# Kernel tuning notes

Measured on AMD Instinct MI355X. Metric: run time of the kernel, lower is better.

## Reference

```python
import jax, jax.numpy as jnp
import numpy as np

NC = 80          # num_classes
REG_MAX = 16
TOPK = 10
IMG = 640
STRIDES = (8, 16, 32)
EPS = 1e-9


def make_anchors(shapes, strides):
    pts, strs = [], []
    for (h, w), s in zip(shapes, strides):
        sx = jnp.arange(w, dtype=jnp.float32)  # grid_cell_offset = 0.0
        sy = jnp.arange(h, dtype=jnp.float32)
        gy, gx = jnp.meshgrid(sy, sx, indexing='ij')
        pts.append(jnp.stack([gx, gy], -1).reshape(-1, 2))
        strs.append(jnp.full((h * w, 1), float(s), dtype=jnp.float32))
    return jnp.concatenate(pts, 0), jnp.concatenate(strs, 0)  # [A,2], [A,1]


def ciou(box1, box2, eps=1e-7):
    # boxes are xyxy, broadcastable; returns CIoU with last dim squeezed
    b1x1, b1y1, b1x2, b1y2 = jnp.split(box1, 4, -1)
    b2x1, b2y1, b2x2, b2y2 = jnp.split(box2, 4, -1)
    w1, h1 = b1x2 - b1x1, b1y2 - b1y1
    w2, h2 = b2x2 - b2x1, b2y2 - b2y1
    inter = (jnp.clip(jnp.minimum(b1x2, b2x2) - jnp.maximum(b1x1, b2x1), 0.0)
             * jnp.clip(jnp.minimum(b1y2, b2y2) - jnp.maximum(b1y1, b2y1), 0.0))
    union = w1 * h1 + w2 * h2 - inter + eps
    iou = inter / union
    cw = jnp.maximum(b1x2, b2x2) - jnp.minimum(b1x1, b2x1)
    ch = jnp.maximum(b1y2, b2y2) - jnp.minimum(b1y1, b2y1)
    c2 = cw ** 2 + ch ** 2 + eps
    rho2 = ((b2x1 + b2x2 - b1x1 - b1x2) ** 2 + (b2y1 + b2y2 - b1y1 - b1y2) ** 2) / 4.0
    v = (4.0 / np.pi ** 2) * (jnp.arctan(w2 / (h2 + eps)) - jnp.arctan(w1 / (h1 + eps))) ** 2
    alpha = jax.lax.stop_gradient(v / (v - iou + (1.0 + eps)))
    return (iou - (rho2 / c2 + v * alpha))[..., 0]


def bbox_decode(anchor_points, pred_distri):
    # distribution-focal decode: softmax over REG_MAX bins, expectation, dist2bbox
    B, A, _ = pred_distri.shape
    pd = pred_distri.reshape(B, A, 4, REG_MAX)
    proj = jnp.arange(REG_MAX, dtype=jnp.float32)
    dist = jnp.einsum('bacr,r->bac', jax.nn.softmax(pd, -1), proj)  # [B,A,4] ltrb
    lt, rb = dist[..., :2], dist[..., 2:]
    return jnp.concatenate([anchor_points - lt, anchor_points + rb], -1)  # xyxy


def assigner(pd_scores, pd_bboxes, anc_points, gt_labels, gt_bboxes, mask_gt,
             alpha=0.5, beta=6.0):
    # pd_scores [B,A,C] (sigmoid), pd_bboxes [B,A,4], gt_* [B,M,...], mask_gt [B,M,1]
    B, A, C = pd_scores.shape
    M = gt_bboxes.shape[1]
    mask_gt = mask_gt.astype(jnp.float32)
    # anchors whose center lies inside each gt box
    lt = anc_points[None, None, :, :] - gt_bboxes[:, :, None, :2]   # [B,M,A,2]
    rb = gt_bboxes[:, :, None, 2:] - anc_points[None, None, :, :]
    mask_in_gts = (jnp.minimum(lt.min(-1), rb.min(-1)) > EPS).astype(jnp.float32)  # [B,M,A]
    mask = mask_in_gts * mask_gt
    # class score of each anchor at the gt's label
    sc = jnp.take_along_axis(pd_scores[:, None, :, :],
                             gt_labels[:, :, None, None].astype(jnp.int32), axis=-1)[..., 0]  # [B,M,A]
    overlaps = jnp.clip(ciou(gt_bboxes[:, :, None, :], pd_bboxes[:, None, :, :]), 0.0) * mask
    bbox_scores = sc * mask
    align_metric = (bbox_scores ** alpha) * (overlaps ** beta)  # [B,M,A]
    # top-k candidates per gt
    _, idxs = jax.lax.top_k(align_metric, TOPK)                 # [B,M,K]
    valid = jnp.broadcast_to(mask_gt > 0, (B, M, TOPK))
    idxs = jnp.where(valid, idxs, 0)
    cnt = jnp.zeros((B * M, A), jnp.float32).at[
        jnp.arange(B * M)[:, None], idxs.reshape(B * M, TOPK)
    ].add(valid.reshape(B * M, TOPK).astype(jnp.float32)).reshape(B, M, A)
    mask_topk = jnp.where(cnt > 1, 0.0, cnt)
    mask_pos = mask_topk * mask_in_gts * mask_gt               # [B,M,A]
    # resolve anchors assigned to multiple gts by max overlap
    fg = mask_pos.sum(1)                                       # [B,A]
    multi = fg[:, None, :] > 1
    is_max = jax.nn.one_hot(overlaps.argmax(1), M, dtype=jnp.float32).transpose(0, 2, 1)
    mask_pos = jnp.where(multi, is_max, mask_pos)
    fg_mask = mask_pos.sum(1)                                  # [B,A]
    tgt_idx = mask_pos.argmax(1)                               # [B,A]
    # gather targets
    flat = tgt_idx + jnp.arange(B)[:, None] * M
    t_labels = jnp.clip(gt_labels.reshape(-1)[flat], 0)        # [B,A]
    t_bboxes = gt_bboxes.reshape(-1, 4)[flat]                  # [B,A,4]
    t_scores = jax.nn.one_hot(t_labels, C, dtype=jnp.float32) * (fg_mask[..., None] > 0)
    # normalize scores by aligned metric
    am = align_metric * mask_pos
    pos_am = am.max(-1, keepdims=True)                         # [B,M,1]
    pos_ov = (overlaps * mask_pos).max(-1, keepdims=True)      # [B,M,1]
    norm = (am * pos_ov / (pos_am + EPS)).max(1)[..., None]    # [B,A,1]
    return t_bboxes, t_scores * norm, fg_mask > 0


def setup_inputs() -> dict:
    key = jax.random.key(0)
    ks = jax.random.split(key, 9)
    B, M = 16, 32
    inp = {
        'cls0': jax.random.normal(ks[0], (B, NC, 80, 80), jnp.float32),
        'cls1': jax.random.normal(ks[1], (B, NC, 40, 40), jnp.float32),
        'cls2': jax.random.normal(ks[2], (B, NC, 20, 20), jnp.float32),
        'reg0': jax.random.normal(ks[3], (B, 4 * REG_MAX, 80, 80), jnp.float32),
        'reg1': jax.random.normal(ks[4], (B, 4 * REG_MAX, 40, 40), jnp.float32),
        'reg2': jax.random.normal(ks[5], (B, 4 * REG_MAX, 20, 20), jnp.float32),
    }
    cxy = jax.random.uniform(ks[6], (B, M, 2), minval=0.1, maxval=0.9)
    wh = jax.random.uniform(ks[7], (B, M, 2), minval=0.02, maxval=0.25)
    inp['boxes'] = jnp.concatenate([cxy, wh], -1)  # normalized cxcywh
    inp['labels'] = jax.random.randint(ks[8], (B, M), 0, NC)
    return inp


def reference(cls0, cls1, cls2, reg0, reg1, reg2, boxes, labels):
    cls_out, reg_out = [cls0, cls1, cls2], [reg0, reg1, reg2]
    B = cls0.shape[0]
    anc, stride_t = make_anchors([r.shape[2:] for r in reg_out], STRIDES)
    pred_scores = jnp.concatenate(
        [c.transpose(0, 2, 3, 1).reshape(B, -1, NC) for c in cls_out], 1)        # [B,A,C]
    pred_distri = jnp.concatenate(
        [r.transpose(0, 2, 3, 1).reshape(B, -1, 4 * REG_MAX) for r in reg_out], 1)
    # gt2xyxy: normalized cxcywh -> pixel xyxy
    cx, cy, w, h = jnp.split(boxes, 4, -1)
    gt_bboxes = jnp.concatenate([(cx - w / 2) * IMG, (cy - h / 2) * IMG,
                                 (cx + w / 2) * IMG, (cy + h / 2) * IMG], -1)
    mask_gt = gt_bboxes.sum(2, keepdims=True) > 0.0
    pred_bboxes = bbox_decode(anc, pred_distri)                                   # anchor units
    sg = jax.lax.stop_gradient
    t_bboxes, t_scores, fg_mask = assigner(
        sg(jax.nn.sigmoid(pred_scores)), sg(pred_bboxes) * stride_t,
        anc * stride_t, labels, gt_bboxes, mask_gt)
    tss = jnp.maximum(t_scores.sum(), 1.0)
    # classification BCE-with-logits
    x, t = pred_scores, t_scores
    bce = jnp.maximum(x, 0.0) - x * t + jnp.log1p(jnp.exp(-jnp.abs(x)))
    l_cls = bce.sum() / tss
    # bbox CIoU loss
    t_bboxes = t_bboxes / stride_t
    weight = t_scores.sum(-1) * fg_mask                                           # [B,A]
    iou = ciou(pred_bboxes, t_bboxes)
    l_iou = ((1.0 - iou) * weight).sum() / tss
    # DFL loss
    tltrb = jnp.clip(jnp.concatenate([anc - t_bboxes[..., :2],
                                      t_bboxes[..., 2:] - anc], -1),
                     0.0, REG_MAX - 1 - 0.01)                                     # [B,A,4]
    logp = jax.nn.log_softmax(pred_distri.reshape(B, -1, 4, REG_MAX), -1)
    tl = jnp.floor(tltrb).astype(jnp.int32)
    wl = (tl + 1).astype(jnp.float32) - tltrb
    lp_tl = jnp.take_along_axis(logp, tl[..., None], -1)[..., 0]
    lp_tr = jnp.take_along_axis(logp, (tl + 1)[..., None], -1)[..., 0]
    dfl = (-(lp_tl * wl + lp_tr * (1.0 - wl))).mean(-1)                           # [B,A]
    l_dfl = (dfl * weight).sum() / tss
    loss = jnp.stack([0.5 * l_cls, 7.5 * l_iou, 1.5 * l_dfl])
    return loss.sum(), loss
```

## Files before the change

### kernel.cpp

```cpp
#include <hip/hip_runtime.h>

#define NB 16
#define NM 32
#define NA 8400
#define NCC 80
#define NREG 64
#define A0 6400
#define A1 1600
#define A2 400
#define CAP 768

#define DEC_BLKS 2100
#define BCE_BLKS 2048
#define PRE_GRID (DEC_BLKS + BCE_BLKS)
#define PL_GRID 525


__device__ __forceinline__ void anch(int a, float& ax, float& ay, float& s, int& lvl, int& p) {
  if (a < A0)            { lvl = 0; p = a;          s = 8.f;  ax = (float)(p % 80); ay = (float)(p / 80); }
  else if (a < A0 + A1)  { lvl = 1; p = a - A0;     s = 16.f; ax = (float)(p % 40); ay = (float)(p / 40); }
  else                   { lvl = 2; p = a - A0 - A1; s = 32.f; ax = (float)(p % 20); ay = (float)(p / 20); }
}

__device__ __forceinline__ float cls_at(const float* c0, const float* c1, const float* c2,
                                        int b, int ch, int a) {
  if (a < A0)           return c0[((size_t)(b * NCC + ch)) * A0 + a];
  if (a < A0 + A1)      return c1[((size_t)(b * NCC + ch)) * A1 + (a - A0)];
  return c2[((size_t)(b * NCC + ch)) * A2 + (a - A0 - A1)];
}

__device__ __forceinline__ float reg_at(const float* r0, const float* r1, const float* r2,
                                        int b, int ch, int lvl, int p) {
  if (lvl == 0) return r0[((size_t)(b * NREG + ch)) * A0 + p];
  if (lvl == 1) return r1[((size_t)(b * NREG + ch)) * A1 + p];
  return r2[((size_t)(b * NREG + ch)) * A2 + p];
}

__device__ __forceinline__ void gtbox(const float* boxes, int b, int m,
                                      float& x1, float& y1, float& x2, float& y2, bool& valid) {
  const float* q = boxes + ((size_t)(b * NM + m)) * 4;
  float cx = q[0], cy = q[1], w = q[2], h = q[3];
  x1 = (cx - w * 0.5f) * 640.f; y1 = (cy - h * 0.5f) * 640.f;
  x2 = (cx + w * 0.5f) * 640.f; y2 = (cy + h * 0.5f) * 640.f;
  valid = (x1 + y1 + x2 + y2) > 0.f;
}

__device__ __forceinline__ float ciou_f(float b1x1, float b1y1, float b1x2, float b1y2,
                                        float b2x1, float b2y1, float b2x2, float b2y2) {
  const float eps = 1e-7f;
  float w1 = b1x2 - b1x1, h1 = b1y2 - b1y1;
  float w2 = b2x2 - b2x1, h2 = b2y2 - b2y1;
  float iw = fmaxf(fminf(b1x2, b2x2) - fmaxf(b1x1, b2x1), 0.f);
  float ih = fmaxf(fminf(b1y2, b2y2) - fmaxf(b1y1, b2y1), 0.f);
  float inter = iw * ih;
  float uni = w1 * h1 + w2 * h2 - inter + eps;
  float iou = inter / uni;
  float cw = fmaxf(b1x2, b2x2) - fminf(b1x1, b2x1);
  float ch = fmaxf(b1y2, b2y2) - fminf(b1y1, b2y1);
  float c2 = cw * cw + ch * ch + eps;
  float dx = b2x1 + b2x2 - b1x1 - b1x2;
  float dy = b2y1 + b2y2 - b1y1 - b1y2;
  float rho2 = (dx * dx + dy * dy) * 0.25f;
  float at = atanf(w2 / (h2 + eps)) - atanf(w1 / (h1 + eps));
  float v = 0.4052847345693511f * at * at;
  float alpha = v / (v - iou + (1.0f + eps));
  return iou - (rho2 / c2 + v * alpha);
}

__device__ __forceinline__ float align_of(float sc, float o) {
  float o2 = o * o, o4 = o2 * o2;
  return sqrtf(sc) * (o2 * o4);
}

__device__ __forceinline__ float softplus_fast(float x) {
  float e = __expf(-fabsf(x));
  return fmaxf(x, 0.f) + __logf(1.f + e);
}


__global__ __launch_bounds__(256) void k_pre2(
    const float* r0, const float* r1, const float* r2,
    const float* c0, const float* c1, const float* c2,
    float* bbf, float* mlsf, int* fgcnt, int* msum,
    unsigned* pos_am, unsigned* pos_ov, double* gt_acc, double* bce_part) {
  __shared__ double sred[256];
  if (blockIdx.x < DEC_BLKS) {
    const int g = blockIdx.x * 256 + threadIdx.x;
    if (g < NB * NA) { fgcnt[g] = 0; msum[g] = 0; }
    if (g < NB * NM) { pos_am[g] = 0u; pos_ov[g] = 0u; }
    if (g < NB * NM * 4) gt_acc[g] = 0.0;

    const int BA = NB * NA;
    const int sd = g / BA;
    const int t  = g - sd * BA;
    int b = t / NA, a = t - (t / NA) * NA;
    float ax, ay, s; int lvl, p;
    anch(a, ax, ay, s, lvl, p);
    const float* rg; int HW;
    if (lvl == 0) { rg = r0; HW = A0; }
    else if (lvl == 1) { rg = r1; HW = A1; }
    else { rg = r2; HW = A2; }
    const float* base = rg + ((size_t)(b * NREG + sd * 16)) * HW + p;
    float xv[16];
#pragma unroll
    for (int r = 0; r < 16; ++r) xv[r] = base[(size_t)r * HW];
    float mx = xv[0];
#pragma unroll
    for (int r = 1; r < 16; ++r) mx = fmaxf(mx, xv[r]);
    float se = 0.f, ws = 0.f;
#pragma unroll
    for (int r = 0; r < 16; ++r) { float e = __expf(xv[r] - mx); se += e; ws += e * (float)r; }
    float dist = ws / se;
    float ml = mx + __logf(se);
    float v;
    if (sd == 0)      v = ax - dist;
    else if (sd == 1) v = ay - dist;
    else if (sd == 2) v = ax + dist;
    else              v = ay + dist;
    bbf[(size_t)t * 4 + sd]  = v;
    mlsf[(size_t)t * 4 + sd] = ml;
  } else {
    const int bce_blk = blockIdx.x - DEC_BLKS;
    const size_t N0 = (size_t)NB * NCC * A0 / 4;
    const size_t N1 = (size_t)NB * NCC * A1 / 4;
    const size_t N2 = (size_t)NB * NCC * A2 / 4;
    const size_t NT = N0 + N1 + N2;
    const float4* f0 = (const float4*)c0;
    const float4* f1 = (const float4*)c1;
    const float4* f2 = (const float4*)c2;
    const size_t i0 = (size_t)bce_blk * 256 + threadIdx.x;
    const size_t stride = (size_t)BCE_BLKS * 256;
    float s0 = 0.f, s1 = 0.f;
    for (size_t i = i0; i < NT; i += stride) {
      float4 v;
      if (i < N0) v = f0[i];
      else if (i < N0 + N1) v = f1[i - N0];
      else v = f2[i - N0 - N1];
      s0 += softplus_fast(v.x) + softplus_fast(v.z);
      s1 += softplus_fast(v.y) + softplus_fast(v.w);
    }
    sred[threadIdx.x] = (double)(s0 + s1);
    __syncthreads();
    for (int off = 128; off; off >>= 1) {
      if (threadIdx.x < off) sred[threadIdx.x] += sred[threadIdx.x + off];
      __syncthreads();
    }
    if (threadIdx.x == 0) bce_part[bce_blk] = sred[0];
  }
}


__global__ __launch_bounds__(256) void k_assign(
    const float* boxes, const int* labels, const float4* bb,
    const float* c0, const float* c1, const float* c2,
    int* fgcnt, int* msum) {
  __shared__ float sv[CAP];
  __shared__ int   si[CAP];
  __shared__ int   s_n;
  const int bm = blockIdx.x;
  const int b = bm / NM, m = bm % NM;
  const int tid = threadIdx.x;
  const int lane = tid & 63;

  float gx1, gy1, gx2, gy2; bool valid;
  gtbox(boxes, b, m, gx1, gy1, gx2, gy2, valid);
  if (!valid) return;
  int lbl = labels[bm]; if (lbl < 0) lbl = 0; if (lbl >= NCC) lbl = NCC - 1;
  if (tid == 0) s_n = 0;
  __syncthreads();

  const int   Ws[3]   = {80, 40, 20};
  const float ss[3]   = {8.f, 16.f, 32.f};
  const int   loff[3] = {0, A0, A0 + A1};
  int rx0[3], ry0[3], rw[3], bc[3];
  int total = 0;
  for (int l = 0; l < 3; ++l) {
    float s = ss[l]; int W = Ws[l];
    int ax0 = (int)floorf((gx1 + 1e-9f) / s);
    int ax1 = (int)ceilf((gx2 - 1e-9f) / s);
    int ay0 = (int)floorf((gy1 + 1e-9f) / s);
    int ay1 = (int)ceilf((gy2 - 1e-9f) / s);
    ax0 = max(ax0, 0); ay0 = max(ay0, 0);
    ax1 = min(ax1, W - 1); ay1 = min(ay1, W - 1);
    rx0[l] = ax0; ry0[l] = ay0;
    rw[l] = max(0, ax1 - ax0 + 1);
    int rhl = max(0, ay1 - ay0 + 1);
    bc[l] = total;
    total += rw[l] * rhl;
  }
  int iters = (total + 255) >> 8;
  for (int it = 0; it < iters; ++it) {
    int idx = it * 256 + tid;
    bool pred = false; float am = 0.f; int a = 0;
    if (idx < total) {
      int l = (idx >= bc[2]) ? 2 : ((idx >= bc[1]) ? 1 : 0);
      int r = idx - bc[l];
      int iy = r / rw[l], ix = r - iy * rw[l];
      int axg = rx0[l] + ix, ayg = ry0[l] + iy;
      a = loff[l] + ayg * Ws[l] + axg;
      float s = ss[l];
      float axp = (float)axg * s, ayp = (float)ayg * s;
      float mn = fminf(fminf(axp - gx1, ayp - gy1), fminf(gx2 - axp, gy2 - ayp));
      if (mn > 1e-9f) {
        pred = true;
        float4 pb = bb[(size_t)b * NA + a];
        float c = ciou_f(gx1, gy1, gx2, gy2, pb.x * s, pb.y * s, pb.z * s, pb.w * s);
        float o = fmaxf(c, 0.f);
        float x = cls_at(c0, c1, c2, b, lbl, a);
        float sc = 1.f / (1.f + expf(-x));
        am = align_of(sc, o);
      }
    }
    unsigned long long mask = __ballot(pred);
    if (mask) {
      int nact = __popcll(mask);
      int leader = __ffsll(mask) - 1;
      int basec = 0;
      if (lane == leader) basec = atomicAdd(&s_n, nact);
      basec = __shfl(basec, leader);
      if (pred) {
        int off = basec + __popcll(mask & ((1ull << lane) - 1ull));
        if (off < CAP) { sv[off] = am; si[off] = a; }
      }
    }
  }
  __syncthreads();
  int n = s_n; if (n > CAP) n = CAP;
  if (n == 0) return;
  if (tid >= 64) return;

  float v[12]; int ix[12];
#pragma unroll
  for (int k = 0; k < 12; ++k) {
    int j = k * 64 + tid;
    bool in = (j < n);
    v[k]  = in ? sv[j] : -2.f;
    ix[k] = in ? si[j] : (1 << 30);
  }
  int cnt = 0;
#pragma unroll
  for (int k = 0; k < 12; ++k) cnt += (v[k] > 0.f) ? 1 : 0;
  for (int o = 32; o; o >>= 1) cnt += __shfl_xor(cnt, o);
  int npos = cnt;

  if (npos > 10) {
    for (int p = 0; p < 10; ++p) {
      float bv = -1.f; int bi = 1 << 30;
#pragma unroll
      for (int k = 0; k < 12; ++k) {
        if (v[k] > bv || (v[k] == bv && ix[k] < bi)) { bv = v[k]; bi = ix[k]; }
      }
      for (int o = 32; o; o >>= 1) {
        float wv = __shfl_xor(bv, o); int wi = __shfl_xor(bi, o);
        if (wv > bv || (wv == bv && wi < bi)) { bv = wv; bi = wi; }
      }
#pragma unroll
      for (int k = 0; k < 12; ++k) if (ix[k] == bi) v[k] = -1.f;
      if (tid == 0) {
        atomicAdd(&fgcnt[(size_t)b * NA + bi], 1);
        atomicAdd(&msum[(size_t)b * NA + bi], m);
      }
    }
  } else {
#pragma unroll
    for (int k = 0; k < 12; ++k) {
      if (v[k] > 0.f) {
        atomicAdd(&fgcnt[(size_t)b * NA + ix[k]], 1);
        atomicAdd(&msum[(size_t)b * NA + ix[k]], m);
      }
    }
    int need = 10 - npos;
    for (int j = tid; j < n; j += 64) {
      if (sv[j] == 0.f) {
        int i = si[j];
        if (i < 10) {
          int pb = 0;
          for (int q = 0; q < n; ++q) pb += (sv[q] > 0.f && si[q] < i) ? 1 : 0;
          if (i - pb < need) {
            atomicAdd(&fgcnt[(size_t)b * NA + i], 1);
            atomicAdd(&msum[(size_t)b * NA + i], m);
          }
        }
      }
    }
  }
}


__global__ __launch_bounds__(256) void k_rp(
    const float* boxes, const int* labels,
    const float4* bb, const float4* mls,
    const float* c0, const float* c1, const float* c2,
    const float* r0, const float* r1, const float* r2,
    const int* fgcnt, const int* msum,
    unsigned* pos_am, unsigned* pos_ov, double* gt_acc) {
  int t = blockIdx.x * 256 + threadIdx.x;
  if (t >= NB * NA) return;
  int fg = fgcnt[t];
  if (fg == 0) return;
  int b = t / NA, a = t % NA;
  float ax, ay, s; int lvl, p;
  anch(a, ax, ay, s, lvl, p);
  float axp = ax * s, ayp = ay * s;
  float4 pb = bb[t];
  float px1 = pb.x * s, py1 = pb.y * s, px2 = pb.z * s, py2 = pb.w * s;
  int asn; float o;
  if (fg == 1) {
    asn = msum[t];
    float gx1, gy1, gx2, gy2; bool valid;
    gtbox(boxes, b, asn, gx1, gy1, gx2, gy2, valid);
    o = fmaxf(ciou_f(gx1, gy1, gx2, gy2, px1, py1, px2, py2), 0.f);
  } else {
    float bv = -1e30f; int bi = 0;
    for (int m = 0; m < NM; ++m) {
      float gx1, gy1, gx2, gy2; bool valid;
      gtbox(boxes, b, m, gx1, gy1, gx2, gy2, valid);
      float om = 0.f;
      if (valid) {
        float mn = fminf(fminf(axp - gx1, ayp - gy1), fminf(gx2 - axp, gy2 - ayp));
        if (mn > 1e-9f)
          om = fmaxf(ciou_f(gx1, gy1, gx2, gy2, px1, py1, px2, py2), 0.f);
      }
      if (om > bv) { bv = om; bi = m; }
    }
    asn = bi; o = bv;
  }
  if (o <= 0.f) return;
  int g = b * NM + asn;
  int lbl = labels[g]; if (lbl < 0) lbl = 0; if (lbl >= NCC) lbl = NCC - 1;
  float x = cls_at(c0, c1, c2, b, lbl, a);
  float sc = 1.f / (1.f + expf(-x));
  float am = align_of(sc, o);
  atomicMax(&pos_am[g], __float_as_uint(am));
  atomicMax(&pos_ov[g], __float_as_uint(o));
  if (am <= 0.f) return;

  float gx1, gy1, gx2, gy2; bool valid;
  gtbox(boxes, b, asn, gx1, gy1, gx2, gy2, valid);
  float inv_s = 1.f / s;
  float tx1 = gx1 * inv_s, ty1 = gy1 * inv_s, tx2 = gx2 * inv_s, ty2 = gy2 * inv_s;
  float iou = ciou_f(pb.x, pb.y, pb.z, pb.w, tx1, ty1, tx2, ty2);
  float4 ml = mls[t];
  float tgt[4] = { ax - tx1, ay - ty1, tx2 - ax, ty2 - ay };
  float mlv[4] = { ml.x, ml.y, ml.z, ml.w };
  float dfl = 0.f;
  for (int sd = 0; sd < 4; ++sd) {
    float tv = fminf(fmaxf(tgt[sd], 0.f), 14.99f);
    float tlf = floorf(tv);
    int tl = (int)tlf;
    float wl = (tlf + 1.f) - tv;
    float xtl = reg_at(r0, r1, r2, b, sd * 16 + tl,     lvl, p);
    float xtr = reg_at(r0, r1, r2, b, sd * 16 + tl + 1, lvl, p);
    dfl += -((xtl - mlv[sd]) * wl + (xtr - mlv[sd]) * (1.f - wl));
  }
  dfl *= 0.25f;
  atomicAdd(&gt_acc[g * 4 + 0], (double)am);
  atomicAdd(&gt_acc[g * 4 + 1], (double)(am * x));
  atomicAdd(&gt_acc[g * 4 + 2], (double)(am * (1.f - iou)));
  atomicAdd(&gt_acc[g * 4 + 3], (double)(am * dfl));
}


__global__ __launch_bounds__(256) void k_final(const double* bce_part, const double* gt_acc,
                                               const unsigned* pos_am, const unsigned* pos_ov,
                                               float* out) {
  const int tid = threadIdx.x;
  double tss = 0.0, sx = 0.0, siou = 0.0, sdfl = 0.0, bce = 0.0;
  for (int g = tid; g < NB * NM; g += 256) {
    float pam = __uint_as_float(pos_am[g]);
    float pov = __uint_as_float(pos_ov[g]);
    double sc = (double)pov / ((double)pam + 1e-9);
    tss  += gt_acc[g * 4 + 0] * sc;
    sx   += gt_acc[g * 4 + 1] * sc;
    siou += gt_acc[g * 4 + 2] * sc;
    sdfl += gt_acc[g * 4 + 3] * sc;
  }
  for (int i = tid; i < BCE_BLKS; i += 256) bce += bce_part[i];
  __shared__ double sred[256];
  double vals[5] = { tss, sx, siou, sdfl, bce };
  double tot[5];
  for (int q = 0; q < 5; ++q) {
    sred[tid] = vals[q];
    __syncthreads();
    for (int off = 128; off; off >>= 1) {
      if (tid < off) sred[tid] += sred[tid + off];
      __syncthreads();
    }
    tot[q] = sred[0];
    __syncthreads();
  }
  if (tid == 0) {
    double t = tot[0]; if (t < 1.0) t = 1.0;
    double l0 = 0.5 * (tot[4] - tot[1]) / t;
    double l1 = 7.5 * tot[2] / t;
    double l2 = 1.5 * tot[3] / t;
    out[0] = (float)(l0 + l1 + l2);
    out[1] = (float)l0;
    out[2] = (float)l1;
    out[3] = (float)l2;
  }
}


extern "C" void kernel_launch(void* const* d_in, const int* in_sizes, int n_in,
                              void* d_out, int out_size, void* d_ws, size_t ws_size,
                              hipStream_t stream) {
  (void)in_sizes; (void)n_in; (void)out_size; (void)ws_size;
  const float* cls0  = (const float*)d_in[0];
  const float* cls1  = (const float*)d_in[1];
  const float* cls2  = (const float*)d_in[2];
  const float* reg0  = (const float*)d_in[3];
  const float* reg1  = (const float*)d_in[4];
  const float* reg2  = (const float*)d_in[5];
  const float* boxes = (const float*)d_in[6];
  const int*   labels = (const int*)d_in[7];
  float* out = (float*)d_out;

  const size_t BA = (size_t)NB * NA;
  const int    BM = NB * NM;

  char* wsb = (char*)d_ws;
  double*   bce_part = (double*)wsb;
  double*   gt_acc   = bce_part + BCE_BLKS;
  unsigned* pos_am   = (unsigned*)(gt_acc + (size_t)BM * 4);
  unsigned* pos_ov   = pos_am + BM;
  int*      fgcnt    = (int*)(pos_ov + BM);
  int*      msum     = fgcnt + BA;
  float*    bbp      = (float*)(msum + BA);
  float*    mlsp     = bbp + BA * 4;

  float4* bb  = (float4*)bbp;
  float4* mls = (float4*)mlsp;

  k_pre2<<<PRE_GRID, 256, 0, stream>>>(reg0, reg1, reg2, cls0, cls1, cls2,
                                       bbp, mlsp, fgcnt, msum, pos_am, pos_ov,
                                       gt_acc, bce_part);
  k_assign<<<BM, 256, 0, stream>>>(boxes, labels, (const float4*)bb,
                                   cls0, cls1, cls2, fgcnt, msum);
  k_rp<<<PL_GRID, 256, 0, stream>>>(boxes, labels, (const float4*)bb, (const float4*)mls,
                                    cls0, cls1, cls2, reg0, reg1, reg2,
                                    fgcnt, msum, pos_am, pos_ov, gt_acc);
  k_final<<<1, 256, 0, stream>>>(bce_part, gt_acc, pos_am, pos_ov, out);
}
```

Baseline: 66.49 us.

## Stage DFL decode through LDS per anchor tile and write float4 outputs

The decode path now has each block handle a 256-anchor tile of one batch and level. It stages the 64 regression channels through shared memory in two 32-channel phases, so each thread computes all four sides and writes bbox and log-sum-exp values as single float4 stores instead of strided scalar stores. Workspace zeroing moves into the BCE blocks. The cost is a 32 KB LDS allocation per block, which can reduce occupancy for the BCE blocks as well, plus extra barriers and idle threads in partial tiles.

```diff
diff --git a/kernel.cpp b/kernel.cpp
--- a/kernel.cpp
+++ b/kernel.cpp
@@ -10,7 +10,8 @@
 #define A2 400
 #define CAP 768
 
-#define DEC_BLKS 2100
+#define TILES_PER_B 34
+#define DEC_BLKS (NB * TILES_PER_B)
 #define BCE_BLKS 2048
 #define PRE_GRID (DEC_BLKS + BCE_BLKS)
 #define PL_GRID 525
@@ -78,49 +79,70 @@
 }
 
 
-__global__ __launch_bounds__(256) void k_pre2(
+__global__ __launch_bounds__(256) void k_pre3(
     const float* r0, const float* r1, const float* r2,
     const float* c0, const float* c1, const float* c2,
-    float* bbf, float* mlsf, int* fgcnt, int* msum,
+    float4* bb4, float4* mls4, int* fgcnt, int* msum,
     unsigned* pos_am, unsigned* pos_ov, double* gt_acc, double* bce_part) {
-  __shared__ double sred[256];
+  __shared__ __align__(8) float lds[32 * 256];
+  const int tid = threadIdx.x;
+
   if (blockIdx.x < DEC_BLKS) {
-    const int g = blockIdx.x * 256 + threadIdx.x;
-    if (g < NB * NA) { fgcnt[g] = 0; msum[g] = 0; }
-    if (g < NB * NM) { pos_am[g] = 0u; pos_ov[g] = 0u; }
-    if (g < NB * NM * 4) gt_acc[g] = 0.0;
-
-    const int BA = NB * NA;
-    const int sd = g / BA;
-    const int t  = g - sd * BA;
-    int b = t / NA, a = t - (t / NA) * NA;
-    float ax, ay, s; int lvl, p;
-    anch(a, ax, ay, s, lvl, p);
-    const float* rg; int HW;
-    if (lvl == 0) { rg = r0; HW = A0; }
-    else if (lvl == 1) { rg = r1; HW = A1; }
-    else { rg = r2; HW = A2; }
-    const float* base = rg + ((size_t)(b * NREG + sd * 16)) * HW + p;
-    float xv[16];
-#pragma unroll
-    for (int r = 0; r < 16; ++r) xv[r] = base[(size_t)r * HW];
-    float mx = xv[0];
-#pragma unroll
-    for (int r = 1; r < 16; ++r) mx = fmaxf(mx, xv[r]);
-    float se = 0.f, ws = 0.f;
-#pragma unroll
-    for (int r = 0; r < 16; ++r) { float e = __expf(xv[r] - mx); se += e; ws += e * (float)r; }
-    float dist = ws / se;
-    float ml = mx + __logf(se);
-    float v;
-    if (sd == 0)      v = ax - dist;
-    else if (sd == 1) v = ay - dist;
-    else if (sd == 2) v = ax + dist;
-    else              v = ay + dist;
-    bbf[(size_t)t * 4 + sd]  = v;
-    mlsf[(size_t)t * 4 + sd] = ml;
+    const int d = blockIdx.x;
+    const int b = d / TILES_PER_B, u = d % TILES_PER_B;
+    int lvl, tile;
+    if (u < 25)      { lvl = 0; tile = u; }
+    else if (u < 32) { lvl = 1; tile = u - 25; }
+    else             { lvl = 2; tile = u - 32; }
+    const int HW   = (lvl == 0) ? A0 : (lvl == 1 ? A1 : A2);
+    const int W    = (lvl == 0) ? 80 : (lvl == 1 ? 40 : 20);
+    const int loff = (lvl == 0) ? 0  : (lvl == 1 ? A0 : A0 + A1);
+    const float* rg = (lvl == 0) ? r0 : (lvl == 1 ? r1 : r2);
+    const int base_p = tile * 256;
+    const int valid  = min(256, HW - base_p);
+    const float* src = rg + (size_t)b * NREG * HW + base_p;
+
+    float dist[4], mlv[4];
+#pragma unroll
+    for (int ph = 0; ph < 2; ++ph) {
+      for (int ch = 0; ch < 32; ++ch) {
+        if (tid < valid)
+          lds[ch * 256 + tid] = src[(size_t)(ph * 32 + ch) * HW + tid];
+      }
+      __syncthreads();
+      if (tid < valid) {
+#pragma unroll
+        for (int sh = 0; sh < 2; ++sh) {
+          const float* col = &lds[(sh * 16) * 256 + tid];
+          float mx = col[0];
+#pragma unroll
+          for (int r = 1; r < 16; ++r) mx = fmaxf(mx, col[r * 256]);
+          float se = 0.f, ws = 0.f;
+#pragma unroll
+          for (int r = 0; r < 16; ++r) {
+            float e = __expf(col[r * 256] - mx);
+            se += e; ws += e * (float)r;
+          }
+          dist[ph * 2 + sh] = ws / se;
+          mlv[ph * 2 + sh]  = mx + __logf(se);
+        }
+      }
+      __syncthreads();
+    }
+    if (tid < valid) {
+      int p = base_p + tid;
+      float ax = (float)(p % W), ay = (float)(p / W);
+      int t = b * NA + loff + p;
+      bb4[t]  = make_float4(ax - dist[0], ay - dist[1], ax + dist[2], ay + dist[3]);
+      mls4[t] = make_float4(mlv[0], mlv[1], mlv[2], mlv[3]);
+    }
   } else {
     const int bce_blk = blockIdx.x - DEC_BLKS;
+    const int gz = bce_blk * 256 + tid;
+    if (gz < NB * NA) { fgcnt[gz] = 0; msum[gz] = 0; }
+    if (gz < NB * NM) { pos_am[gz] = 0u; pos_ov[gz] = 0u; }
+    if (gz < NB * NM * 4) gt_acc[gz] = 0.0;
+
     const size_t N0 = (size_t)NB * NCC * A0 / 4;
     const size_t N1 = (size_t)NB * NCC * A1 / 4;
     const size_t N2 = (size_t)NB * NCC * A2 / 4;
@@ -128,7 +150,7 @@
     const float4* f0 = (const float4*)c0;
     const float4* f1 = (const float4*)c1;
     const float4* f2 = (const float4*)c2;
-    const size_t i0 = (size_t)bce_blk * 256 + threadIdx.x;
+    const size_t i0 = (size_t)bce_blk * 256 + tid;
     const size_t stride = (size_t)BCE_BLKS * 256;
     float s0 = 0.f, s1 = 0.f;
     for (size_t i = i0; i < NT; i += stride) {
@@ -139,13 +161,14 @@
       s0 += softplus_fast(v.x) + softplus_fast(v.z);
       s1 += softplus_fast(v.y) + softplus_fast(v.w);
     }
-    sred[threadIdx.x] = (double)(s0 + s1);
+    double* sred = (double*)lds;
+    sred[tid] = (double)(s0 + s1);
     __syncthreads();
     for (int off = 128; off; off >>= 1) {
-      if (threadIdx.x < off) sred[threadIdx.x] += sred[threadIdx.x + off];
+      if (tid < off) sred[tid] += sred[tid + off];
       __syncthreads();
     }
-    if (threadIdx.x == 0) bce_part[bce_blk] = sred[0];
+    if (tid == 0) bce_part[bce_blk] = sred[0];
   }
 }
 
@@ -432,8 +455,8 @@
   float4* bb  = (float4*)bbp;
   float4* mls = (float4*)mlsp;
 
-  k_pre2<<<PRE_GRID, 256, 0, stream>>>(reg0, reg1, reg2, cls0, cls1, cls2,
-                                       bbp, mlsp, fgcnt, msum, pos_am, pos_ov,
+  k_pre3<<<PRE_GRID, 256, 0, stream>>>(reg0, reg1, reg2, cls0, cls1, cls2,
+                                       bb, mls, fgcnt, msum, pos_am, pos_ov,
                                        gt_acc, bce_part);
   k_assign<<<BM, 256, 0, stream>>>(boxes, labels, (const float4*)bb,
                                    cls0, cls1, cls2, fgcnt, msum);
```

Result: faster. 64.58 us (-2.9%).
